# Optimization experiments

Measured on AMD Instinct MI355X. Metric: run time of the kernel, lower is better.

The kernel has to match this reference:

```python
import jax, jax.numpy as jnp
import numpy as np

DIM_IN, DIM, BS, H, W = 128, 64, 32, 64, 64
G, K = 5, 3          # KAN grid intervals and spline degree
EPS = 1e-5           # BatchNorm eps


def conv2d(x, w, b, groups=1, pad=0):
    # x: [B,C,H,W], w: [O, C//groups, kh, kw]
    y = jax.lax.conv_general_dilated(
        x, w, window_strides=(1, 1), padding=[(pad, pad), (pad, pad)],
        dimension_numbers=('NCHW', 'OIHW', 'NCHW'), feature_group_count=groups)
    return y + b[None, :, None, None]


def bn(x, g, b, m, v):
    # inference-mode BatchNorm2d
    inv = jax.lax.rsqrt(v + EPS)
    return g[None, :, None, None] * (x - m[None, :, None, None]) * inv[None, :, None, None] + b[None, :, None, None]


def make_grid():
    # extended knot vector over [-1,1], G intervals, degree K: G+2K+1 knots
    h = 2.0 / G
    t = jnp.arange(-K, G + K + 1, dtype=jnp.float32) * h - 1.0
    return jnp.broadcast_to(t, (DIM, G + 2 * K + 1))


def bspline_basis(x, t, k):
    # Cox-de Boor recursion. x: [N,in], t: [in, G+2k+1] -> B: [N,in,G+k]
    xe = x[..., None]
    B = ((xe >= t[:, :-1]) & (xe < t[:, 1:])).astype(x.dtype)
    for p in range(1, k + 1):
        B = ((xe - t[:, :-(p + 1)]) / (t[:, p:-1] - t[:, :-(p + 1)])) * B[..., :-1] \
          + ((t[:, p + 1:] - xe) / (t[:, p + 1:] - t[:, 1:-p])) * B[..., 1:]
    return B


def kan_forward(xk, coef, scale_base, scale_sp, kan_bias):
    # single KANLayer [dim -> dim]: silu residual branch + spline branch + node bias
    t = make_grid()
    B = bspline_basis(xk, t, K)                      # [N, in, G+K]
    y_base = jax.nn.silu(xk) @ scale_base            # [N, out]
    y_sp = jnp.einsum('nij,ioj->no', B, coef * scale_sp[:, :, None])
    return y_base + y_sp + kan_bias


def setup_inputs() -> dict:
    key = jax.random.key(0)
    ks = jax.random.split(key, 24)
    rn = lambda k, s, sc=0.05: jax.random.normal(k, s, jnp.float32) * sc
    return {
        'x': jax.random.normal(ks[0], (BS, DIM_IN, H, W), jnp.float32),
        'reduce_w': rn(ks[1], (DIM, DIM_IN, 1, 1), 0.1), 'reduce_b': rn(ks[2], (DIM,)),
        'dw_w': rn(ks[3], (DIM, 1, 7, 7), 0.1), 'dw_b': rn(ks[4], (DIM,)),
        'dw_g': 1.0 + rn(ks[5], (DIM,)), 'dw_beta': rn(ks[6], (DIM,)),
        'dw_m': rn(ks[7], (DIM,)), 'dw_v': 0.5 + jax.random.uniform(ks[8], (DIM,)),
        'f2_w': rn(ks[9], (DIM, DIM, 1, 1), 0.1), 'f2_b': rn(ks[10], (DIM,)),
        'coef': rn(ks[11], (DIM, DIM, G + K), 0.1),
        'scale_base': 1.0 / np.sqrt(DIM) + rn(ks[12], (DIM, DIM)),
        'scale_sp': 1.0 + rn(ks[13], (DIM, DIM)),
        'kan_bias': rn(ks[14], (DIM,)),
        'g_w': rn(ks[15], (DIM, DIM, 1, 1), 0.1), 'g_b': rn(ks[16], (DIM,)),
        'g_g': 1.0 + rn(ks[17], (DIM,)), 'g_beta': rn(ks[18], (DIM,)),
        'g_m': rn(ks[19], (DIM,)), 'g_v': 0.5 + jax.random.uniform(ks[20], (DIM,)),
        'dw2_w': rn(ks[21], (DIM, 1, 7, 7), 0.1), 'dw2_b': rn(ks[22], (DIM,)),
    }


def reference(x, reduce_w, reduce_b, dw_w, dw_b, dw_g, dw_beta, dw_m, dw_v,
              f2_w, f2_b, coef, scale_base, scale_sp, kan_bias,
              g_w, g_b, g_g, g_beta, g_m, g_v, dw2_w, dw2_b):
    x = conv2d(x, reduce_w, reduce_b)                       # dim_reduce 1x1
    inp = x
    xd = bn(conv2d(x, dw_w, dw_b, groups=DIM, pad=3), dw_g, dw_beta, dw_m, dw_v)  # 7x7 dwconv + BN
    bs, dim, h, w = xd.shape
    xk = xd.transpose(0, 2, 3, 1).reshape(bs * h * w, dim)  # tokenwise view
    x1 = kan_forward(xk, coef, scale_base, scale_sp, kan_bias)
    x1 = x1.reshape(bs, h, w, dim).transpose(0, 3, 1, 2)    # back to NCHW
    x2 = conv2d(xd, f2_w, f2_b)                             # f2 1x1
    y = x1 * x2                                             # elementwise gate
    y = bn(conv2d(y, g_w, g_b), g_g, g_beta, g_m, g_v)      # g 1x1 + BN
    y = conv2d(y, dw2_w, dw2_b, groups=DIM, pad=3)          # dwconv2 7x7
    return inp + y
```

## Files before the change

kernel.cpp:

```cpp
#include <hip/hip_runtime.h>
#include <hip/hip_bf16.h>

#define BSZ 32
#define CIN 128
#define CD 64
#define HH 64
#define WW 64
#define PLANE (HH * WW)
#define NPIX (BSZ * HH * WW)
#define NB 8
#define BN_EPS 1e-5f

typedef __attribute__((ext_vector_type(8))) short short8v;
typedef __attribute__((ext_vector_type(4))) float f32x4;
typedef __attribute__((ext_vector_type(4))) unsigned int u32x4;

static __device__ __forceinline__ short f2bf(float f) {
    __hip_bfloat16 h = __float2bfloat16(f);
    return __builtin_bit_cast(short, h);
}
static __device__ __forceinline__ unsigned int cvtpk(float lo, float hi) {
    unsigned int r;
    asm("v_cvt_pk_bf16_f32 %0, %1, %2" : "=v"(r) : "v"(lo), "v"(hi));
    return r;
}
static __device__ __forceinline__ u32x4 basisD(float v) {
    const float tt = (v + 2.2f) * 2.5f;
    const float fi = floorf(tt);
    const int i0 = (int)fi;
    const float u = tt - fi;
    const bool inr = (tt >= 0.0f) && (tt < 11.0f);
    const float u2 = u * u, u3 = u2 * u;
    const float t1 = 1.f - u;
    const float w0 = (1.f / 6.f) * t1 * t1 * t1;
    const float w3 = (1.f / 6.f) * u3;
    const float w1 = fmaf(0.5f, u3, 2.f / 3.f) - u2;
    const float w2 = 1.f - w0 - w1 - w3;
    unsigned W01 = cvtpk(w0, w1);
    unsigned W23 = cvtpk(w2, w3);
    if (!inr) { W01 = 0u; W23 = 0u; }
    const unsigned long long P =
        ((unsigned long long)W23 << 32) | (unsigned long long)W01;
    const int t = (i0 - 3) << 4;
    const unsigned long long S1 = P << (t & 63);
    const unsigned long long S2 = P >> ((64 - t) & 63);
    const bool c1 = (unsigned)t < 64u;
    const bool c2 = t < 0;
    const bool c3 = t >= 64;
    const bool c5 = t > 0;
    const unsigned long long lo = c1 ? S1 : (c2 ? S2 : 0ULL);
    const unsigned long long hi = c3 ? S1 : ((c1 && c5) ? S2 : 0ULL);
    u32x4 D;
    D.x = (unsigned)lo;
    D.y = (unsigned)(lo >> 32);
    D.z = (unsigned)hi;
    D.w = (unsigned)(hi >> 32);
    return D;
}
static __device__ __forceinline__ void gather_frags(
    const unsigned* __restrict__ pad, int s3, int hi, int m,
    short8v& f0, short8v& f1)
{
    unsigned q[8];
#pragma unroll
    for (int e = 0; e < 8; ++e) q[e] = pad[(s3 * 32 + 8 * hi + e) * 17 + m];
#pragma unroll
    for (int qi = 0; qi < 4; ++qi) {
        ((unsigned*)&f0)[qi] = (q[2 * qi] & 0xffffu) | (q[2 * qi + 1] << 16);
        ((unsigned*)&f1)[qi] = (q[2 * qi] >> 16) | (q[2 * qi + 1] & 0xffff0000u);
    }
}

__global__ __launch_bounds__(256) void k_prep(
    const float* __restrict__ coef, const float* __restrict__ ssp,
    const float* __restrict__ sb, const float* __restrict__ f2w,
    const float* __restrict__ reduce_w, const float* __restrict__ g_w,
    const float* __restrict__ dw_g, const float* __restrict__ dw_beta,
    const float* __restrict__ dw_m, const float* __restrict__ dw_v,
    const float* __restrict__ dw_b, const float* __restrict__ g_g,
    const float* __restrict__ g_beta, const float* __restrict__ g_m,
    const float* __restrict__ g_v, const float* __restrict__ g_b,
    short* __restrict__ W1f, short* __restrict__ W2f,
    short* __restrict__ WRf, short* __restrict__ WGf,
    float* __restrict__ cbuf)
{
    const int idx = blockIdx.x * 256 + threadIdx.x;
    if (idx < 36864) {
        const int e = idx & 7, l = (idx >> 3) & 63, c = (idx >> 9) & 3, s = idx >> 11;
        const int k = s * 32 + ((l >> 4) << 3) + e;
        const int j = (c << 4) + (l & 15);
        float v;
        if (k < 512) {
            const int i = k >> 3, t = k & 7;
            v = coef[(i * 64 + j) * 8 + t] * ssp[i * 64 + j];
        } else {
            v = sb[(k - 512) * 64 + j];
        }
        W1f[idx] = f2bf(v);
    } else if (idx < 45056) {
        const int f = idx - 36864;
        const int e = f & 7, l = (f >> 3) & 63, c = (f >> 9) & 3, s = f >> 11;
        const int k = s * 32 + ((l >> 4) << 3) + e;
        const int j = (c << 4) + (l & 15);
        W2f[f] = f2bf(f2w[j * 64 + k]);
    } else if (idx < 53248) {
        const int f = idx - 45056;
        const int e = f & 7, l = (f >> 3) & 63, c = (f >> 9) & 3, s = f >> 11;
        const int k = s * 32 + ((l >> 4) << 3) + e;
        const int j = (c << 4) + (l & 15);
        WRf[f] = f2bf(reduce_w[j * CIN + k]);
    } else if (idx < 57344) {
        const int f = idx - 53248;
        const int e = f & 7, l = (f >> 3) & 63, c = (f >> 9) & 3, s = f >> 11;
        const int k = s * 32 + ((l >> 4) << 3) + e;
        const int j = (c << 4) + (l & 15);
        WGf[f] = f2bf(g_w[j * 64 + k]);
    } else if (idx < 57600) {
        const int q = (idx - 57344) >> 6, c = idx & 63;
        if (q == 0) cbuf[c] = dw_g[c] * rsqrtf(dw_v[c] + BN_EPS);
        else if (q == 1) {
            float sc = dw_g[c] * rsqrtf(dw_v[c] + BN_EPS);
            cbuf[64 + c] = (dw_b[c] - dw_m[c]) * sc + dw_beta[c];
        } else if (q == 2) cbuf[128 + c] = g_g[c] * rsqrtf(g_v[c] + BN_EPS);
        else {
            float sc = g_g[c] * rsqrtf(g_v[c] + BN_EPS);
            cbuf[192 + c] = (g_b[c] - g_m[c]) * sc + g_beta[c];
        }
    }
}

__global__ __launch_bounds__(256) void k_reduce_mfma(
    const float* __restrict__ x, const short* __restrict__ WRf,
    const float* __restrict__ bias, float* __restrict__ out)
{
    __shared__ __align__(16) char smem[34048];
    short* As = (short*)smem;
    float* Osh = (float*)smem;
    const int bid = blockIdx.x;
    const int b = bid >> 5, h0 = (bid & 31) * 2;
    const int tid = threadIdx.x;
    const float* xb = x + (size_t)b * CIN * PLANE + h0 * WW;
#pragma unroll 1
    for (int p = 0; p < 64; ++p) {
        const int idx = tid + (p << 8);
        const int c = idx >> 7, rt = idx & 127;
        const float v = xb[(size_t)c * PLANE + rt];
        const int s = c >> 5, g = (c >> 3) & 3, e = c & 7;
        const int mt = rt >> 4, m = rt & 15;
        As[((mt * 4 + s) * 64 + (((g << 4) | m) ^ (s & 7))) * 8 + e] = f2bf(v);
    }
    __syncthreads();
    const int cw = tid >> 6, l = tid & 63;
    f32x4 acc[8];
#pragma unroll
    for (int i = 0; i < 8; ++i) acc[i] = (f32x4){0.f, 0.f, 0.f, 0.f};
#pragma unroll 1
    for (int s = 0; s < 4; ++s) {
        const short8v bfr = *(const short8v*)&WRf[((s * 4 + cw) * 64 + l) * 8];
        const int lx = l ^ (s & 7);
#pragma unroll
        for (int mt = 0; mt < 8; ++mt) {
            const short8v a = *(const short8v*)&As[((mt * 4 + s) * 64 + lx) * 8];
            acc[mt] = __builtin_amdgcn_mfma_f32_16x16x32_bf16(a, bfr, acc[mt], 0, 0, 0);
        }
    }
    __syncthreads();
    const int j = (cw << 4) + (l & 15);
    const float bj = bias[j];
    const int rb = (l >> 4) << 2;
#pragma unroll
    for (int mt = 0; mt < 8; ++mt)
#pragma unroll
        for (int r = 0; r < 4; ++r)
            Osh[j * 133 + mt * 16 + rb + r] = acc[mt][r] + bj;
    __syncthreads();
    float* ob = out + (size_t)b * CD * PLANE + h0 * WW;
#pragma unroll 1
    for (int p = 0; p < 32; ++p) {
        const int idx = tid + (p << 8);
        const int jj = idx >> 7, rt = idx & 127;
        ob[(size_t)jj * PLANE + rt] = Osh[jj * 133 + rt];
    }
}

template<bool RESID>
__global__ __launch_bounds__(256) void k_dwconv(
    const float* __restrict__ in, const float* __restrict__ filt,
    const float* __restrict__ sc, const float* __restrict__ shv,
    const float* __restrict__ resid, float* __restrict__ out)
{
    const int bid = blockIdx.x;
    const int b = bid >> 6, c4 = (bid >> 2) & 15, strip = bid & 3;
    const int H0 = strip << 4;
    const int c = c4 * 4 + (threadIdx.x >> 6);
    const int lane = threadIdx.x & 63;
    const size_t pbase = ((size_t)b * CD + c) * PLANE;
    const float* plane = in + pbase;
    const float* wp = filt + c * 49;
    float K[49];
#pragma unroll
    for (int q = 0; q < 49; ++q) K[q] = wp[q];
    const float scl = RESID ? 1.f : sc[c];
    const float shf = shv[c];
    const float* rplane = RESID ? (resid + pbase) : nullptr;
    float* oplane = out + pbase;

    float acc[7] = {0.f, 0.f, 0.f, 0.f, 0.f, 0.f, 0.f};
#pragma unroll
    for (int rr = 0; rr < 22; ++rr) {
        const int ra = H0 + rr - 3;
        float rowv = 0.f;
        if (ra >= 0 && ra < 64) rowv = plane[ra * 64 + lane];
        float sh[7];
        sh[3] = rowv;
#pragma unroll
        for (int d = 1; d <= 3; ++d) {
            float tp = __shfl(rowv, lane + d);
            sh[3 + d] = (lane + d < 64) ? tp : 0.f;
            float tm = __shfl(rowv, lane - d);
            sh[3 - d] = (lane - d >= 0) ? tm : 0.f;
        }
#pragma unroll
        for (int dy = 0; dy < 7; ++dy) {
            const int o = rr - dy;
            if (o >= 0 && o < 16) {
                const int slot = o % 7;
#pragma unroll
                for (int dx = 0; dx < 7; ++dx)
                    acc[slot] = fmaf(sh[dx], K[dy * 7 + dx], acc[slot]);
            }
        }
        const int done = rr - 6;
        if (done >= 0 && done < 16) {
            const int slot = done % 7;
            const int h = H0 + done;
            float val;
            if (RESID) val = acc[slot] + shf + rplane[h * 64 + lane];
            else       val = acc[slot] * scl + shf;
            oplane[h * 64 + lane] = val;
            acc[slot] = 0.f;
        }
    }
}

__global__ __launch_bounds__(256) void k_kan_fused(
    const float* __restrict__ xd, const short* __restrict__ W1f,
    const short* __restrict__ W2f, const short* __restrict__ WGf,
    const float* __restrict__ kb, const float* __restrict__ f2b,
    const float* __restrict__ gs, const float* __restrict__ gsh,
    float* __restrict__ z)
{
    __shared__ __align__(16) short As1[2 * 18 * 64 * 8];
    __shared__ __align__(16) short As2[2 * 2 * 64 * 8];
    __shared__ unsigned yPad[64 * 17];
    const int tid = threadIdx.x;
    const int tg0 = blockIdx.x * 32;
    const int bb = tg0 >> 12, pix0 = tg0 & 4095;
    const float* xb = xd + (size_t)bb * CD * PLANE + pix0;
    float* zb = z + (size_t)bb * CD * PLANE + pix0;
    const int tkn = tid & 31;
    const int w5 = tid >> 5;
    const int mt = tkn >> 4, m = tkn & 15;

    float vf[8], sf[8];
#pragma unroll
    for (int p = 0; p < 8; ++p) {
        const int c = w5 * 8 + p;
        const float v = xb[(size_t)c * PLANE + tkn];
        vf[p] = v;
        sf[p] = v * __builtin_amdgcn_rcpf(1.0f + __expf(-v));
        const u32x4 D = basisD(v);
        const int s = w5 * 2 + (p >> 2);
        const int phys = (((p & 3) << 4) | m) ^ (s & 7);
        *(u32x4*)&As1[((mt * 18 + s) * 64 + phys) * 8] = D;
    }
    {
        short8v vpk, spk;
#pragma unroll
        for (int q = 0; q < 4; ++q) {
            ((unsigned*)&vpk)[q] = cvtpk(vf[2 * q], vf[2 * q + 1]);
            ((unsigned*)&spk)[q] = cvtpk(sf[2 * q], sf[2 * q + 1]);
        }
        const int slot = ((w5 & 3) << 4) | m;
        const int s2 = 16 + (w5 >> 2);
        *(short8v*)&As1[((mt * 18 + s2) * 64 + (slot ^ (s2 & 7))) * 8] = spk;
        const int s3 = w5 >> 2;
        *(short8v*)&As2[((mt * 2 + s3) * 64 + (slot ^ (s3 & 7))) * 8] = vpk;
    }
    __syncthreads();

    const int cw = tid >> 6, l = tid & 63;
    const int hi = l >> 4;
    const int j = (cw << 4) + (l & 15);
    const int mq = l & 15;
    const int rb = hi << 2;
    const float kbj = kb[j], f2bj = f2b[j];
    const float sj = gs[j], hj = gsh[j];

    f32x4 accA0 = {0.f,0.f,0.f,0.f}, accA1 = {0.f,0.f,0.f,0.f};
    f32x4 accB0 = {0.f,0.f,0.f,0.f}, accB1 = {0.f,0.f,0.f,0.f};
#pragma unroll
    for (int s = 0; s < 18; ++s) {
        const short8v bfr = *(const short8v*)&W1f[((s * 4 + cw) * 64 + l) * 8];
        const short8v a0 = *(const short8v*)&As1[((0 * 18 + s) * 64 + (l ^ (s & 7))) * 8];
        const short8v a1 = *(const short8v*)&As1[((1 * 18 + s) * 64 + (l ^ (s & 7))) * 8];
        accA0 = __builtin_amdgcn_mfma_f32_16x16x32_bf16(a0, bfr, accA0, 0, 0, 0);
        accA1 = __builtin_amdgcn_mfma_f32_16x16x32_bf16(a1, bfr, accA1, 0, 0, 0);
    }
#pragma unroll
    for (int s = 0; s < 2; ++s) {
        const short8v bfr = *(const short8v*)&W2f[((s * 4 + cw) * 64 + l) * 8];
        const short8v a0 = *(const short8v*)&As2[((0 * 2 + s) * 64 + (l ^ s)) * 8];
        const short8v a1 = *(const short8v*)&As2[((1 * 2 + s) * 64 + (l ^ s)) * 8];
        accB0 = __builtin_amdgcn_mfma_f32_16x16x32_bf16(a0, bfr, accB0, 0, 0, 0);
        accB1 = __builtin_amdgcn_mfma_f32_16x16x32_bf16(a1, bfr, accB1, 0, 0, 0);
    }

#pragma unroll
    for (int r = 0; r < 4; ++r) {
        const float ya = (accA0[r] + kbj) * (accB0[r] + f2bj);
        const float yb = (accA1[r] + kbj) * (accB1[r] + f2bj);
        yPad[j * 17 + rb + r] = cvtpk(ya, yb);
    }
    __syncthreads();

    f32x4 acc30 = {0.f,0.f,0.f,0.f}, acc31 = {0.f,0.f,0.f,0.f};
#pragma unroll
    for (int s3 = 0; s3 < 2; ++s3) {
        const short8v bfr = *(const short8v*)&WGf[((s3 * 4 + cw) * 64 + l) * 8];
        short8v f0, f1;
        gather_frags(yPad, s3, hi, mq, f0, f1);
        acc30 = __builtin_amdgcn_mfma_f32_16x16x32_bf16(f0, bfr, acc30, 0, 0, 0);
        acc31 = __builtin_amdgcn_mfma_f32_16x16x32_bf16(f1, bfr, acc31, 0, 0, 0);
    }

    f32x4 o0, o1;
#pragma unroll
    for (int r = 0; r < 4; ++r) {
        o0[r] = acc30[r] * sj + hj;
        o1[r] = acc31[r] * sj + hj;
    }
    *(f32x4*)&zb[(size_t)j * PLANE + rb] = o0;
    *(f32x4*)&zb[(size_t)j * PLANE + 16 + rb] = o1;
}

extern "C" void kernel_launch(void* const* d_in, const int* in_sizes, int n_in,
                              void* d_out, int out_size, void* d_ws, size_t ws_size,
                              hipStream_t stream)
{
    (void)in_sizes; (void)n_in; (void)out_size; (void)ws_size;
    const float* x        = (const float*)d_in[0];
    const float* reduce_w = (const float*)d_in[1];
    const float* reduce_b = (const float*)d_in[2];
    const float* dw_w     = (const float*)d_in[3];
    const float* dw_b     = (const float*)d_in[4];
    const float* dw_g     = (const float*)d_in[5];
    const float* dw_beta  = (const float*)d_in[6];
    const float* dw_m     = (const float*)d_in[7];
    const float* dw_v     = (const float*)d_in[8];
    const float* f2_w     = (const float*)d_in[9];
    const float* f2_b     = (const float*)d_in[10];
    const float* coef     = (const float*)d_in[11];
    const float* sbase    = (const float*)d_in[12];
    const float* ssp      = (const float*)d_in[13];
    const float* kbias    = (const float*)d_in[14];
    const float* g_w      = (const float*)d_in[15];
    const float* g_b      = (const float*)d_in[16];
    const float* g_g      = (const float*)d_in[17];
    const float* g_beta   = (const float*)d_in[18];
    const float* g_m      = (const float*)d_in[19];
    const float* g_v      = (const float*)d_in[20];
    const float* dw2_w    = (const float*)d_in[21];
    const float* dw2_b    = (const float*)d_in[22];
    float* out = (float*)d_out;

    const size_t NEL = (size_t)BSZ * CD * PLANE;
    short* W1f = (short*)d_ws;
    short* W2f = W1f + 36864;
    short* WRf = W2f + 8192;
    short* WGf = WRf + 8192;
    float* cbuf = (float*)((char*)d_ws + 115200);
    float* inp = (float*)((char*)d_ws + 131072);
    float* xdb = inp + NEL;
    float* z   = xdb + NEL;

    k_prep<<<225, 256, 0, stream>>>(coef, ssp, sbase, f2_w, reduce_w, g_w,
                                    dw_g, dw_beta, dw_m, dw_v, dw_b,
                                    g_g, g_beta, g_m, g_v, g_b,
                                    W1f, W2f, WRf, WGf, cbuf);
    k_reduce_mfma<<<BSZ * 32, 256, 0, stream>>>(x, WRf, reduce_b, inp);
    k_dwconv<false><<<BSZ * 16 * 4, 256, 0, stream>>>(inp, dw_w, cbuf, cbuf + 64, nullptr, xdb);
    k_kan_fused<<<NPIX / 32, 256, 0, stream>>>(xdb, W1f, W2f, WGf, kbias, f2_b,
                                               cbuf + 128, cbuf + 192, z);
    k_dwconv<true><<<BSZ * 16 * 4, 256, 0, stream>>>(z, dw2_w, nullptr, dw2_b, inp, out);
}
```

Measured before the change: 103.3 us.

## Store intermediate activations in bf16 to halve memory traffic

Changes the three intermediate buffers (reduced input, dwconv+BN output, gated KAN output) from fp32 to bf16. Producers pack their results with a bf16 convert and consumers widen on load. The pipeline is memory-bound, so this is meant to cut global read and write bytes between stages. The cost is lower precision, including on the residual input added at the end, which may raise error against the reference.

```diff
diff --git a/kernel.cpp b/kernel.cpp
--- a/kernel.cpp
+++ b/kernel.cpp
@@ -18,6 +18,9 @@
 static __device__ __forceinline__ short f2bf(float f) {
     __hip_bfloat16 h = __float2bfloat16(f);
     return __builtin_bit_cast(short, h);
+}
+static __device__ __forceinline__ float bf2f(unsigned short u) {
+    return __builtin_bit_cast(float, (unsigned)u << 16);
 }
 static __device__ __forceinline__ unsigned int cvtpk(float lo, float hi) {
     unsigned int r;
@@ -131,7 +134,7 @@
 
 __global__ __launch_bounds__(256) void k_reduce_mfma(
     const float* __restrict__ x, const short* __restrict__ WRf,
-    const float* __restrict__ bias, float* __restrict__ out)
+    const float* __restrict__ bias, unsigned short* __restrict__ out)
 {
     __shared__ __align__(16) char smem[34048];
     short* As = (short*)smem;
@@ -174,20 +177,21 @@
         for (int r = 0; r < 4; ++r)
             Osh[j * 133 + mt * 16 + rb + r] = acc[mt][r] + bj;
     __syncthreads();
-    float* ob = out + (size_t)b * CD * PLANE + h0 * WW;
+    unsigned short* ob = out + (size_t)b * CD * PLANE + h0 * WW;
 #pragma unroll 1
-    for (int p = 0; p < 32; ++p) {
+    for (int p = 0; p < 16; ++p) {
         const int idx = tid + (p << 8);
-        const int jj = idx >> 7, rt = idx & 127;
-        ob[(size_t)jj * PLANE + rt] = Osh[jj * 133 + rt];
+        const int jj = idx >> 6, rt2 = (idx & 63) * 2;
+        const unsigned pk = cvtpk(Osh[jj * 133 + rt2], Osh[jj * 133 + rt2 + 1]);
+        *(unsigned*)&ob[(size_t)jj * PLANE + rt2] = pk;
     }
 }
 
 template<bool RESID>
 __global__ __launch_bounds__(256) void k_dwconv(
-    const float* __restrict__ in, const float* __restrict__ filt,
+    const unsigned short* __restrict__ in, const float* __restrict__ filt,
     const float* __restrict__ sc, const float* __restrict__ shv,
-    const float* __restrict__ resid, float* __restrict__ out)
+    const unsigned short* __restrict__ resid, void* __restrict__ outv)
 {
     const int bid = blockIdx.x;
     const int b = bid >> 6, c4 = (bid >> 2) & 15, strip = bid & 3;
@@ -195,22 +199,23 @@
     const int c = c4 * 4 + (threadIdx.x >> 6);
     const int lane = threadIdx.x & 63;
     const size_t pbase = ((size_t)b * CD + c) * PLANE;
-    const float* plane = in + pbase;
+    const unsigned short* plane = in + pbase;
     const float* wp = filt + c * 49;
     float K[49];
 #pragma unroll
     for (int q = 0; q < 49; ++q) K[q] = wp[q];
     const float scl = RESID ? 1.f : sc[c];
     const float shf = shv[c];
-    const float* rplane = RESID ? (resid + pbase) : nullptr;
-    float* oplane = out + pbase;
+    const unsigned short* rplane = RESID ? (resid + pbase) : nullptr;
+    float* oplane_f = RESID ? ((float*)outv + pbase) : nullptr;
+    unsigned short* oplane_h = RESID ? nullptr : ((unsigned short*)outv + pbase);
 
     float acc[7] = {0.f, 0.f, 0.f, 0.f, 0.f, 0.f, 0.f};
 #pragma unroll
     for (int rr = 0; rr < 22; ++rr) {
         const int ra = H0 + rr - 3;
         float rowv = 0.f;
-        if (ra >= 0 && ra < 64) rowv = plane[ra * 64 + lane];
+        if (ra >= 0 && ra < 64) rowv = bf2f(plane[ra * 64 + lane]);
         float sh[7];
         sh[3] = rowv;
 #pragma unroll
@@ -234,21 +239,24 @@
         if (done >= 0 && done < 16) {
             const int slot = done % 7;
             const int h = H0 + done;
-            float val;
-            if (RESID) val = acc[slot] + shf + rplane[h * 64 + lane];
-            else       val = acc[slot] * scl + shf;
-            oplane[h * 64 + lane] = val;
+            if (RESID) {
+                oplane_f[h * 64 + lane] =
+                    acc[slot] + shf + bf2f(rplane[h * 64 + lane]);
+            } else {
+                oplane_h[h * 64 + lane] =
+                    (unsigned short)(unsigned short)f2bf(acc[slot] * scl + shf);
+            }
             acc[slot] = 0.f;
         }
     }
 }
 
 __global__ __launch_bounds__(256) void k_kan_fused(
-    const float* __restrict__ xd, const short* __restrict__ W1f,
+    const unsigned short* __restrict__ xd, const short* __restrict__ W1f,
     const short* __restrict__ W2f, const short* __restrict__ WGf,
     const float* __restrict__ kb, const float* __restrict__ f2b,
     const float* __restrict__ gs, const float* __restrict__ gsh,
-    float* __restrict__ z)
+    unsigned short* __restrict__ z)
 {
     __shared__ __align__(16) short As1[2 * 18 * 64 * 8];
     __shared__ __align__(16) short As2[2 * 2 * 64 * 8];
@@ -256,8 +264,8 @@
     const int tid = threadIdx.x;
     const int tg0 = blockIdx.x * 32;
     const int bb = tg0 >> 12, pix0 = tg0 & 4095;
-    const float* xb = xd + (size_t)bb * CD * PLANE + pix0;
-    float* zb = z + (size_t)bb * CD * PLANE + pix0;
+    const unsigned short* xb = xd + (size_t)bb * CD * PLANE + pix0;
+    unsigned short* zb = z + (size_t)bb * CD * PLANE + pix0;
     const int tkn = tid & 31;
     const int w5 = tid >> 5;
     const int mt = tkn >> 4, m = tkn & 15;
@@ -266,7 +274,7 @@
 #pragma unroll
     for (int p = 0; p < 8; ++p) {
         const int c = w5 * 8 + p;
-        const float v = xb[(size_t)c * PLANE + tkn];
+        const float v = bf2f(xb[(size_t)c * PLANE + tkn]);
         vf[p] = v;
         sf[p] = v * __builtin_amdgcn_rcpf(1.0f + __expf(-v));
         const u32x4 D = basisD(v);
@@ -334,14 +342,13 @@
         acc31 = __builtin_amdgcn_mfma_f32_16x16x32_bf16(f1, bfr, acc31, 0, 0, 0);
     }
 
-    f32x4 o0, o1;
-#pragma unroll
-    for (int r = 0; r < 4; ++r) {
-        o0[r] = acc30[r] * sj + hj;
-        o1[r] = acc31[r] * sj + hj;
-    }
-    *(f32x4*)&zb[(size_t)j * PLANE + rb] = o0;
-    *(f32x4*)&zb[(size_t)j * PLANE + 16 + rb] = o1;
+    uint2 p0, p1;
+    p0.x = cvtpk(acc30[0] * sj + hj, acc30[1] * sj + hj);
+    p0.y = cvtpk(acc30[2] * sj + hj, acc30[3] * sj + hj);
+    p1.x = cvtpk(acc31[0] * sj + hj, acc31[1] * sj + hj);
+    p1.y = cvtpk(acc31[2] * sj + hj, acc31[3] * sj + hj);
+    *(uint2*)&zb[(size_t)j * PLANE + rb] = p0;
+    *(uint2*)&zb[(size_t)j * PLANE + 16 + rb] = p1;
 }
 
 extern "C" void kernel_launch(void* const* d_in, const int* in_sizes, int n_in,
@@ -380,9 +387,9 @@
     short* WRf = W2f + 8192;
     short* WGf = WRf + 8192;
     float* cbuf = (float*)((char*)d_ws + 115200);
-    float* inp = (float*)((char*)d_ws + 131072);
-    float* xdb = inp + NEL;
-    float* z   = xdb + NEL;
+    unsigned short* inp = (unsigned short*)((char*)d_ws + 131072);
+    unsigned short* xdb = inp + NEL;
+    unsigned short* z   = xdb + NEL;
 
     k_prep<<<225, 256, 0, stream>>>(coef, ssp, sbase, f2_w, reduce_w, g_w,
                                     dw_g, dw_beta, dw_m, dw_v, dw_b,
```

New measurement: 103.9 us. Within noise of the previous version (+0.6%).
